# Kernel tuning notes

Hardware: AMD Instinct MI355X
Metric: run time of the kernel (lower is better)

## Reference

```python
import jax, jax.numpy as jnp
import numpy as np

# --- Mamba2Simple hyperparams (derived from init_kwargs) ---
D_MODEL = 2048
D_STATE = 128
HEADDIM = 64
EXPAND = 2
D_CONV = 4
NGROUPS = 1
CHUNK = 256
EPS = 1e-5
D_INNER = EXPAND * D_MODEL            # 4096
NHEADS = D_INNER // HEADDIM           # 64
CONV_DIM = D_INNER + 2 * NGROUPS * D_STATE          # 4352
D_IN_PROJ = 2 * D_INNER + 2 * NGROUPS * D_STATE + NHEADS  # 8512


def setup_inputs() -> dict:
    key = jax.random.key(0)
    ks = jax.random.split(key, 9)
    B, L = 2, 2048
    x = jax.random.normal(ks[0], (B, L, D_MODEL), jnp.float32)
    w_in = jax.random.normal(ks[1], (D_MODEL, D_IN_PROJ), jnp.float32) * (D_MODEL ** -0.5)
    conv_w = jax.random.normal(ks[2], (CONV_DIM, D_CONV), jnp.float32) * 0.2
    conv_b = jnp.zeros((CONV_DIM,), jnp.float32)
    dt_bias = jax.random.uniform(ks[3], (NHEADS,), jnp.float32, -4.0, -1.0)
    # A in [1, 16] per official init -> A_log = log(A)
    A_log = jnp.log(jax.random.uniform(ks[4], (NHEADS,), jnp.float32, 1.0, 16.0))
    D = jnp.ones((NHEADS,), jnp.float32)
    norm_w = jnp.ones((D_INNER,), jnp.float32)
    w_out = jax.random.normal(ks[5], (D_INNER, D_MODEL), jnp.float32) * (D_INNER ** -0.5)
    return {"x": x, "w_in": w_in, "conv_w": conv_w, "conv_b": conv_b,
            "dt_bias": dt_bias, "A_log": A_log, "D": D, "norm_w": norm_w, "w_out": w_out}


def _segsum(a):
    # a: (..., T) -> (..., T, T) with out[i, j] = sum_{k=j+1..i} a[k] for j<=i else -inf
    T = a.shape[-1]
    cs = jnp.cumsum(a, axis=-1)
    d = cs[..., :, None] - cs[..., None, :]
    mask = jnp.tril(jnp.ones((T, T), dtype=bool))
    return jnp.where(mask, d, -jnp.inf)


def _ssd(X, A, Bm, Cm):
    # X: (b, l, h, p) already multiplied by dt; A: (b, l, h) = dt*A_cont
    # Bm, Cm: (b, l, n)  (ngroups=1, broadcast over heads)
    b, l, h, p = X.shape
    n = Bm.shape[-1]
    c = l // CHUNK
    X = X.reshape(b, c, CHUNK, h, p)
    A = A.reshape(b, c, CHUNK, h).transpose(0, 3, 1, 2)      # (b, h, c, q)
    Bm = Bm.reshape(b, c, CHUNK, n)
    Cm = Cm.reshape(b, c, CHUNK, n)
    A_cs = jnp.cumsum(A, axis=-1)                             # (b, h, c, q)
    Lmat = jnp.exp(_segsum(A))                                # (b, h, c, q, q)
    # intra-chunk (diagonal block) output
    Y_diag = jnp.einsum("bcln,bcsn,bhcls,bcshp->bclhp", Cm, Bm, Lmat, X)
    # per-chunk final states
    decay_states = jnp.exp(A_cs[..., -1:] - A_cs)             # (b, h, c, q)
    states = jnp.einsum("bcln,bhcl,bclhp->bchpn", Bm, decay_states, X)
    # inter-chunk recurrence
    A_last = jnp.pad(A_cs[..., -1], ((0, 0), (0, 0), (1, 0)))  # (b, h, c+1)
    decay_chunk = jnp.exp(_segsum(A_last))                     # (b, h, c+1, c+1)
    states = jnp.concatenate([jnp.zeros_like(states[:, :1]), states], axis=1)
    states = jnp.einsum("bhzc,bchpn->bzhpn", decay_chunk, states)[:, :-1]
    # state -> output contribution
    Y_off = jnp.einsum("bchpn,bcln,bhcl->bclhp", states, Cm, jnp.exp(A_cs))
    return (Y_diag + Y_off).reshape(b, l, h, p)


def _mamba2(x, w_in, conv_w, conv_b, dt_bias, A_log, D, norm_w, w_out):
    B, L, _ = x.shape
    zxbcdt = jnp.einsum("bld,de->ble", x, w_in)               # (B, L, 8512)
    z = zxbcdt[..., :D_INNER]
    xBC = zxbcdt[..., D_INNER:D_INNER + CONV_DIM]
    dt = zxbcdt[..., D_INNER + CONV_DIM:]                      # (B, L, H)
    dt = jax.nn.softplus(dt + dt_bias)
    # causal depthwise conv1d + silu
    xp = jnp.pad(xBC, ((0, 0), (D_CONV - 1, 0), (0, 0)))
    acc = conv_b
    xBC = sum(conv_w[:, k] * xp[:, k:k + L, :] for k in range(D_CONV)) + conv_b
    xBC = jax.nn.silu(xBC)
    xh = xBC[..., :D_INNER].reshape(B, L, NHEADS, HEADDIM)
    Bm = xBC[..., D_INNER:D_INNER + NGROUPS * D_STATE]         # (B, L, N) since ngroups=1
    Cm = xBC[..., D_INNER + NGROUPS * D_STATE:]                # (B, L, N)
    A = -jnp.exp(A_log)                                        # (H,)
    y = _ssd(xh * dt[..., None], dt * A, Bm, Cm)               # (B, L, H, P)
    y = y + xh * D[None, None, :, None]                        # skip term
    y = y.reshape(B, L, D_INNER)
    # gated RMSNorm (norm_before_gate=False): normalize(y * silu(z)) * weight
    y = y * jax.nn.silu(z)
    y = y * jax.lax.rsqrt(jnp.mean(y * y, axis=-1, keepdims=True) + EPS) * norm_w
    return jnp.einsum("ble,ed->bld", y, w_out)


def reference(x, w_in, conv_w, conv_b, dt_bias, A_log, D, norm_w, w_out):
    return x + _mamba2(x, w_in, conv_w, conv_b, dt_bias, A_log, D, norm_w, w_out)
```

## Files before the change

### kernel.cpp

```cpp
#include <hip/hip_runtime.h>
#include <math.h>

#define DEV __device__ __forceinline__

typedef __attribute__((ext_vector_type(4))) float f32x4;
typedef __attribute__((ext_vector_type(4))) unsigned short u16x4;
typedef __attribute__((ext_vector_type(8))) unsigned short u16x8;
typedef __attribute__((ext_vector_type(8))) __bf16 bfv8;

DEV unsigned short f2bf(float f) {
  unsigned u = __builtin_bit_cast(unsigned, f);
  u = (u + 0x7FFFu + ((u >> 16) & 1u)) >> 16;
  return (unsigned short)u;
}
DEV float bf2f(unsigned short h) {
  unsigned u = ((unsigned)h) << 16;
  return __builtin_bit_cast(float, u);
}

DEV f32x4 mfma16(u16x8 a, u16x8 b, f32x4 c) {
  return __builtin_amdgcn_mfma_f32_16x16x32_bf16(
      __builtin_bit_cast(bfv8, a), __builtin_bit_cast(bfv8, b), c, 0, 0, 0);
}

DEV void gload_lds16(const unsigned short* g, unsigned short* s) {
  __builtin_amdgcn_global_load_lds(
      (const __attribute__((address_space(1))) void*)g,
      (__attribute__((address_space(3))) void*)s, 16, 0, 0);
}

template <int N>
DEV void vmcnt_wait() {
  if constexpr (N == 0) asm volatile("s_waitcnt vmcnt(0)" ::: "memory");
  else if constexpr (N == 2) asm volatile("s_waitcnt vmcnt(2)" ::: "memory");
  else if constexpr (N == 3) asm volatile("s_waitcnt vmcnt(3)" ::: "memory");
  else if constexpr (N == 4) asm volatile("s_waitcnt vmcnt(4)" ::: "memory");
  else if constexpr (N == 6) asm volatile("s_waitcnt vmcnt(6)" ::: "memory");
  else if constexpr (N == 8) asm volatile("s_waitcnt vmcnt(8)" ::: "memory");
}

template <int BM, int BN, int MODE>
__global__ __launch_bounds__(512, 2) void gemm_p(
    const unsigned short* __restrict__ A, const unsigned short* __restrict__ Bt,
    int K, unsigned short* __restrict__ o_z, unsigned short* __restrict__ o_xbc,
    float* __restrict__ o_dt, float* __restrict__ o_c,
    const float* __restrict__ resid) {
  constexpr int LA = BM / 128, LB = BN / 128, L = LA + LB;
  constexpr int MF = BM / 32, NF = BN / 64, MH = MF / 2;
  __shared__ __align__(16) unsigned short As[3][BM * 32];
  __shared__ __align__(16) unsigned short Bs[3][BN * 32];
  const int tid = threadIdx.x;
  const int lane = tid & 63, w = tid >> 6;
  const int l16 = lane & 15, lq = lane >> 4;
  const int wr = w >> 2, wc = w & 3;
  const int nwg = gridDim.x * gridDim.y;
  int lin = blockIdx.y * gridDim.x + blockIdx.x;
  lin = (lin & 7) * (nwg >> 3) + (lin >> 3);
  const int m0 = (lin / gridDim.x) * BM, n0 = (lin % gridDim.x) * BN;
  const int lrow = lane >> 2;
  const int gq = (lane & 3) ^ ((lrow >> 1) & 3);
  const int cq = lq ^ ((l16 >> 1) & 3);

  const unsigned short* Ag = A + (size_t)(m0 + lrow) * K + gq * 8;
  const unsigned short* Bg = Bt + (size_t)(n0 + lrow) * K + gq * 8;

  f32x4 acc[MF][NF] = {};
  u16x8 bf[NF];

  auto stageA = [&](int bi, int kt) {
#pragma unroll
    for (int i = 0; i < LA; ++i) {
      const int rb = (w + i * 8) * 16;
      gload_lds16(Ag + (size_t)rb * K + kt * 32, &As[bi][rb * 32]);
    }
  };
  auto stageB = [&](int bi, int kt) {
#pragma unroll
    for (int i = 0; i < LB; ++i) {
      const int rb = (w + i * 8) * 16;
      gload_lds16(Bg + (size_t)rb * K + kt * 32, &Bs[bi][rb * 32]);
    }
  };

  const int nt = K / 32;
  stageA(0, 0); stageB(0, 0);
  stageA(1, 1); stageB(1, 1);
  vmcnt_wait<L>();
  __builtin_amdgcn_s_barrier();

  for (int k = 0; k < nt; ++k) {
    const int cb = k % 3;
    const bool st = (k + 2) < nt;
    const int pb = st ? (k + 2) % 3 : 0;
    u16x8 af[MH];
#pragma unroll
    for (int mf = 0; mf < MH; ++mf)
      af[mf] = *(const u16x8*)(&As[cb][(wr * (BM / 2) + mf * 16 + l16) * 32 + cq * 8]);
#pragma unroll
    for (int nf = 0; nf < NF; ++nf)
      bf[nf] = *(const u16x8*)(&Bs[cb][(wc * (BN / 4) + nf * 16 + l16) * 32 + cq * 8]);
    if (st) stageA(pb, k + 2);
    asm volatile("" ::: "memory");
    __builtin_amdgcn_s_barrier();
    __builtin_amdgcn_s_setprio(1);
#pragma unroll
    for (int mf = 0; mf < MH; ++mf)
#pragma unroll
      for (int nf = 0; nf < NF; ++nf)
        acc[mf][nf] = mfma16(af[mf], bf[nf], acc[mf][nf]);
    __builtin_amdgcn_s_setprio(0);
    asm volatile("" ::: "memory");
    __builtin_amdgcn_s_barrier();
#pragma unroll
    for (int mf = 0; mf < MH; ++mf)
      af[mf] = *(const u16x8*)(&As[cb][(wr * (BM / 2) + (MH + mf) * 16 + l16) * 32 + cq * 8]);
    if (st) stageB(pb, k + 2);
    asm volatile("" ::: "memory");
    __builtin_amdgcn_s_barrier();
    __builtin_amdgcn_s_setprio(1);
#pragma unroll
    for (int mf = 0; mf < MH; ++mf)
#pragma unroll
      for (int nf = 0; nf < NF; ++nf)
        acc[MH + mf][nf] = mfma16(af[mf], bf[nf], acc[MH + mf][nf]);
    __builtin_amdgcn_s_setprio(0);
    if (k + 1 < nt) {
      if (st) vmcnt_wait<L>();
      else vmcnt_wait<0>();
    }
    asm volatile("" ::: "memory");
    __builtin_amdgcn_s_barrier();
  }

#pragma unroll
  for (int mf = 0; mf < MF; ++mf) {
#pragma unroll
    for (int nf = 0; nf < NF; ++nf) {
      const int col = n0 + wc * (BN / 4) + nf * 16 + l16;
#pragma unroll
      for (int r = 0; r < 4; ++r) {
        const int row = m0 + wr * (BM / 2) + mf * 16 + lq * 4 + r;
        float v = acc[mf][nf][r];
        if constexpr (MODE == 0) {
          if (col < 4096) o_z[(size_t)row * 4096 + col] = f2bf(v);
          else if (col < 8448) o_xbc[(size_t)row * 4352 + (col - 4096)] = f2bf(v);
          else if (col < 8512) o_dt[(size_t)row * 64 + (col - 8448)] = v;
        } else {
          size_t idx = (size_t)row * 2048 + col;
          o_c[idx] = v + resid[idx];
        }
      }
    }
  }
}

__global__ __launch_bounds__(256) void convert_bf16(
    const float* __restrict__ in, unsigned short* __restrict__ out) {
  const size_t i = ((size_t)blockIdx.x * 256 + threadIdx.x) * 8;
  f32x4 a = *(const f32x4*)(in + i);
  f32x4 b = *(const f32x4*)(in + i + 4);
  u16x8 o;
#pragma unroll
  for (int j = 0; j < 4; ++j) { o[j] = f2bf(a[j]); o[j + 4] = f2bf(b[j]); }
  *(u16x8*)(out + i) = o;
}

__global__ __launch_bounds__(256) void transpose_conv(
    const float* __restrict__ in, unsigned short* __restrict__ out, int R,
    int C) {
  __shared__ __align__(16) unsigned short T[64][72];
  const int c0 = blockIdx.x * 64, r0 = blockIdx.y * 64;
  const int tid = threadIdx.x;
#pragma unroll
  for (int it = 0; it < 4; ++it) {
    int r = it * 16 + (tid >> 4);
    int c = (tid & 15) * 4;
    f32x4 v = {0.f, 0.f, 0.f, 0.f};
    if (c0 + c < C) v = *(const f32x4*)(in + (size_t)(r0 + r) * C + c0 + c);
#pragma unroll
    for (int j = 0; j < 4; ++j) T[c + j][r] = f2bf(v[j]);
  }
  __syncthreads();
  const int nr = tid >> 2, kc = (tid & 3) * 16;
  u16x8 a = *(const u16x8*)(&T[nr][kc]);
  u16x8 b = *(const u16x8*)(&T[nr][kc + 8]);
  unsigned short* o = out + (size_t)(c0 + nr) * R + r0 + kc;
  *(u16x8*)o = a;
  *(u16x8*)(o + 8) = b;
}

__global__ __launch_bounds__(256) void conv_kernel(
    const unsigned short* __restrict__ raw, const float* __restrict__ cw,
    const float* __restrict__ cb, unsigned short* __restrict__ xbc) {
  const int ch4 = blockIdx.x * 256 + threadIdx.x;
  if (ch4 >= 1088) return;
  const int ch = ch4 * 4;
  const int row = blockIdx.y;
  const int l = row & 2047;
  f32x4 acc = *(const f32x4*)(cb + ch);
  f32x4 w0 = *(const f32x4*)(cw + ch * 4);
  f32x4 w1 = *(const f32x4*)(cw + ch * 4 + 4);
  f32x4 w2 = *(const f32x4*)(cw + ch * 4 + 8);
  f32x4 w3 = *(const f32x4*)(cw + ch * 4 + 12);
#pragma unroll
  for (int k = 0; k < 4; ++k) {
    int ls = l - 3 + k;
    if (ls >= 0) {
      u16x4 v = *(const u16x4*)(raw + (size_t)(row - 3 + k) * 4352 + ch);
      acc[0] += w0[k] * bf2f(v[0]);
      acc[1] += w1[k] * bf2f(v[1]);
      acc[2] += w2[k] * bf2f(v[2]);
      acc[3] += w3[k] * bf2f(v[3]);
    }
  }
  u16x4 o;
#pragma unroll
  for (int j = 0; j < 4; ++j) {
    float s = acc[j] / (1.0f + __expf(-acc[j]));
    o[j] = f2bf(s);
  }
  *(u16x4*)(xbc + (size_t)row * 4352 + ch) = o;
}

__global__ __launch_bounds__(256) void dt_kernel(
    float* __restrict__ dtb, const float* __restrict__ dt_bias,
    const float* __restrict__ A_log, float* __restrict__ Acs) {
  __shared__ float s[256];
  const int blk = blockIdx.x;
  const int c = blk & 7, h = (blk >> 3) & 63, b = blk >> 9;
  const int t = threadIdx.x;
  const int row = b * 2048 + c * 256 + t;
  float xv = dtb[(size_t)row * 64 + h] + dt_bias[h];
  float dt = (xv > 20.0f) ? xv : log1pf(__expf(xv));
  dtb[(size_t)row * 64 + h] = dt;
  float a = dt * (-__expf(A_log[h]));
  s[t] = a;
  __syncthreads();
  for (int off = 1; off < 256; off <<= 1) {
    float v = (t >= off) ? s[t - off] : 0.0f;
    __syncthreads();
    s[t] += v;
    __syncthreads();
  }
  Acs[((size_t)((b * 64 + h) * 8 + c)) * 256 + t] = s[t];
}

__global__ __launch_bounds__(256) void g_kernel(
    const unsigned short* __restrict__ xbc, float* __restrict__ G) {
  const int bc = blockIdx.y;
  const int i0 = (blockIdx.x >> 2) * 64, j0 = (blockIdx.x & 3) * 64;
  const int tid = threadIdx.x;
  const int lane = tid & 63, w = tid >> 6;
  const int l16 = lane & 15, lq = lane >> 4;
  const unsigned short* base = xbc + (size_t)bc * 256 * 4352;
  f32x4 acc[4] = {};
#pragma unroll
  for (int ks = 0; ks < 4; ++ks) {
    int nb = ks * 32 + lq * 8;
    u16x8 af = *(const u16x8*)(base + (size_t)(i0 + w * 16 + l16) * 4352 + 4224 + nb);
#pragma unroll
    for (int jf = 0; jf < 4; ++jf) {
      u16x8 bb = *(const u16x8*)(base + (size_t)(j0 + jf * 16 + l16) * 4352 + 4096 + nb);
      acc[jf] = mfma16(af, bb, acc[jf]);
    }
  }
  float* Gt = G + (size_t)bc * 65536;
#pragma unroll
  for (int jf = 0; jf < 4; ++jf)
#pragma unroll
    for (int r = 0; r < 4; ++r)
      Gt[(i0 + w * 16 + lq * 4 + r) * 256 + j0 + jf * 16 + l16] = acc[jf][r];
}

__global__ __launch_bounds__(512) void ssd_states(
    const unsigned short* __restrict__ xbc, const float* __restrict__ dtb,
    const float* __restrict__ Acs, unsigned short* __restrict__ statesb) {
  __shared__ __align__(16) unsigned short Xt[64 * 264];
  __shared__ __align__(16) unsigned short BmT[128 * 72];
  __shared__ float As_s[256];
  const int h = blockIdx.x, c = blockIdx.y, b = blockIdx.z;
  const int tid = threadIdx.x;
  const int lane = tid & 63, w = tid >> 6;
  const int l16 = lane & 15, lq = lane >> 4;
  const int row0 = b * 2048 + c * 256;

  if (tid < 256) As_s[tid] = Acs[((size_t)((b * 64 + h) * 8 + c)) * 256 + tid];
#pragma unroll
  for (int it = 0; it < 2; ++it) {
    int pb = tid & 15;
    int tb = it * 32 + (tid >> 4);
    float rr[4][4];
#pragma unroll
    for (int i = 0; i < 4; ++i) {
      int row = row0 + tb * 4 + i;
      u16x4 v = *(const u16x4*)(xbc + (size_t)row * 4352 + h * 64 + pb * 4);
      float dtv = dtb[(size_t)row * 64 + h];
#pragma unroll
      for (int j = 0; j < 4; ++j) rr[i][j] = bf2f(v[j]) * dtv;
    }
#pragma unroll
    for (int j = 0; j < 4; ++j) {
      u16x4 hh = {f2bf(rr[0][j]), f2bf(rr[1][j]), f2bf(rr[2][j]), f2bf(rr[3][j])};
      *(u16x4*)(&Xt[(pb * 4 + j) * 264 + tb * 4]) = hh;
    }
  }
  __syncthreads();

  f32x4 accS[4] = {};
  const float Alast = As_s[255];
  for (int part = 0; part < 4; ++part) {
    if (part) __syncthreads();
    {
      int nb = tid & 31;
      int tb = tid >> 5;
      float rr[4][4];
#pragma unroll
      for (int i = 0; i < 4; ++i) {
        int t = part * 64 + tb * 4 + i;
        int row = row0 + t;
        float dec = __expf(Alast - As_s[t]);
        u16x4 v = *(const u16x4*)(xbc + (size_t)row * 4352 + 4096 + nb * 4);
#pragma unroll
        for (int j = 0; j < 4; ++j) rr[i][j] = bf2f(v[j]) * dec;
      }
#pragma unroll
      for (int j = 0; j < 4; ++j) {
        u16x4 hh = {f2bf(rr[0][j]), f2bf(rr[1][j]), f2bf(rr[2][j]), f2bf(rr[3][j])};
        *(u16x4*)(&BmT[(nb * 4 + j) * 72 + tb * 4]) = hh;
      }
    }
    __syncthreads();
#pragma unroll
    for (int ks = 0; ks < 2; ++ks) {
      int toff = ks * 32 + lq * 8;
      u16x8 af = *(const u16x8*)(&BmT[(w * 16 + l16) * 72 + toff]);
#pragma unroll
      for (int pf = 0; pf < 4; ++pf) {
        u16x8 bfr = *(const u16x8*)(&Xt[(pf * 16 + l16) * 264 + part * 64 + toff]);
        accS[pf] = mfma16(af, bfr, accS[pf]);
      }
    }
  }
  unsigned short* Sp = statesb + (size_t)((b * 8 + c) * 64 + h) * 8192;
#pragma unroll
  for (int pf = 0; pf < 4; ++pf) {
    u16x4 hh = {f2bf(accS[pf][0]), f2bf(accS[pf][1]), f2bf(accS[pf][2]),
                f2bf(accS[pf][3])};
    *(u16x4*)(&Sp[(pf * 16 + l16) * 128 + w * 16 + lq * 4]) = hh;
  }
}

__global__ __launch_bounds__(256) void scan_states(
    const unsigned short* __restrict__ statesb, const float* __restrict__ Acs,
    unsigned short* __restrict__ prefix) {
  const int h = blockIdx.x, b = blockIdx.y;
  const int tid = threadIdx.x;
  const int p = tid >> 2, nq = (tid & 3) * 32;
  float S[32];
#pragma unroll
  for (int i = 0; i < 32; ++i) S[i] = 0.0f;
  for (int cc = 0; cc < 8; ++cc) {
    size_t base = (size_t)((b * 8 + cc) * 64 + h) * 8192 + p * 128 + nq;
#pragma unroll
    for (int j = 0; j < 4; ++j) {
      u16x8 hh;
#pragma unroll
      for (int k = 0; k < 8; ++k) hh[k] = f2bf(S[j * 8 + k]);
      *(u16x8*)(prefix + base + j * 8) = hh;
    }
    float eAl = __expf(Acs[((size_t)((b * 64 + h) * 8 + cc)) * 256 + 255]);
#pragma unroll
    for (int j = 0; j < 4; ++j) {
      u16x8 v = *(const u16x8*)(statesb + base + j * 8);
#pragma unroll
      for (int k = 0; k < 8; ++k) S[j * 8 + k] = eAl * S[j * 8 + k] + bf2f(v[k]);
    }
  }
}

__global__ __launch_bounds__(512) void ssd_main(
    const unsigned short* __restrict__ xbc, const float* __restrict__ dtb,
    const float* __restrict__ Acs, const float* __restrict__ G,
    const unsigned short* __restrict__ prefix, const float* __restrict__ Dv,
    unsigned short* __restrict__ y) {
  __shared__ __align__(16) unsigned short Xt[64 * 264];
  __shared__ float As_s[256];
  const int h = blockIdx.x, c = blockIdx.y, b = blockIdx.z;
  const int tid = threadIdx.x;
  const int lane = tid & 63, w = tid >> 6;
  const int l16 = lane & 15, lq = lane >> 4;
  const int row0 = b * 2048 + c * 256;

  if (tid < 256) As_s[tid] = Acs[((size_t)((b * 64 + h) * 8 + c)) * 256 + tid];
#pragma unroll
  for (int it = 0; it < 2; ++it) {
    int pb = tid & 15;
    int tb = it * 32 + (tid >> 4);
    float rr[4][4];
#pragma unroll
    for (int i = 0; i < 4; ++i) {
      int row = row0 + tb * 4 + i;
      u16x4 v = *(const u16x4*)(xbc + (size_t)row * 4352 + h * 64 + pb * 4);
      float dtv = dtb[(size_t)row * 64 + h];
#pragma unroll
      for (int j = 0; j < 4; ++j) rr[i][j] = bf2f(v[j]) * dtv;
    }
#pragma unroll
    for (int j = 0; j < 4; ++j) {
      u16x4 hh = {f2bf(rr[0][j]), f2bf(rr[1][j]), f2bf(rr[2][j]), f2bf(rr[3][j])};
      *(u16x4*)(&Xt[(pb * 4 + j) * 264 + tb * 4]) = hh;
    }
  }
  __syncthreads();

  f32x4 acc[2][4] = {};
  const float* Gt = G + (size_t)(b * 8 + c) * 65536;
  for (int ks = 0; ks < 8; ++ks) {
    const int tb = ks * 32 + lq * 8;
    u16x8 bfr[4];
#pragma unroll
    for (int pf = 0; pf < 4; ++pf)
      bfr[pf] = *(const u16x8*)(&Xt[(pf * 16 + l16) * 264 + tb]);
#pragma unroll
    for (int mf = 0; mf < 2; ++mf) {
      const int i = w * 32 + mf * 16 + l16;
      const float ai = As_s[i];
      const float* gp = Gt + i * 256 + tb;
      f32x4 g0 = *(const f32x4*)gp;
      f32x4 g1 = *(const f32x4*)(gp + 4);
      u16x8 af;
#pragma unroll
      for (int jj = 0; jj < 8; ++jj) {
        int j = tb + jj;
        float g = (jj < 4) ? g0[jj] : g1[jj - 4];
        float v = (i >= j) ? g * __expf(ai - As_s[j]) : 0.0f;
        af[jj] = f2bf(v);
      }
#pragma unroll
      for (int pf = 0; pf < 4; ++pf)
        acc[mf][pf] = mfma16(af, bfr[pf], acc[mf][pf]);
    }
  }
  const unsigned short* Pf = prefix + (size_t)((b * 8 + c) * 64 + h) * 8192;
  for (int ks = 0; ks < 4; ++ks) {
    const int nb = ks * 32 + lq * 8;
    u16x8 bfr[4];
#pragma unroll
    for (int pf = 0; pf < 4; ++pf)
      bfr[pf] = *(const u16x8*)(Pf + (size_t)(pf * 16 + l16) * 128 + nb);
#pragma unroll
    for (int mf = 0; mf < 2; ++mf) {
      const int i = w * 32 + mf * 16 + l16;
      const float eAi = __expf(As_s[i]);
      u16x8 cv = *(const u16x8*)(xbc + (size_t)(row0 + i) * 4352 + 4224 + nb);
      u16x8 af;
#pragma unroll
      for (int jj = 0; jj < 8; ++jj) af[jj] = f2bf(bf2f(cv[jj]) * eAi);
#pragma unroll
      for (int pf = 0; pf < 4; ++pf)
        acc[mf][pf] = mfma16(af, bfr[pf], acc[mf][pf]);
    }
  }
  const float Dh = Dv[h];
#pragma unroll
  for (int mf = 0; mf < 2; ++mf) {
#pragma unroll
    for (int r = 0; r < 4; ++r) {
      int t = w * 32 + mf * 16 + lq * 4 + r;
      size_t row = (size_t)(row0 + t);
#pragma unroll
      for (int pf = 0; pf < 4; ++pf) {
        int p = pf * 16 + l16;
        float xh = bf2f(xbc[row * 4352 + h * 64 + p]);
        y[row * 4096 + h * 64 + p] = f2bf(acc[mf][pf][r] + Dh * xh);
      }
    }
  }
}

__global__ __launch_bounds__(256) void norm_kernel(
    unsigned short* __restrict__ y, const unsigned short* __restrict__ zbf,
    const float* __restrict__ nw) {
  const int row = blockIdx.x, tid = threadIdx.x;
  unsigned short* yr = y + (size_t)row * 4096;
  const unsigned short* zr = zbf + (size_t)row * 4096;
  float vals[16];
  float ss = 0.0f;
#pragma unroll
  for (int i = 0; i < 2; ++i) {
    int cb = i * 2048 + tid * 8;
    u16x8 yv = *(const u16x8*)(yr + cb);
    u16x8 zv = *(const u16x8*)(zr + cb);
#pragma unroll
    for (int j = 0; j < 8; ++j) {
      float z = bf2f(zv[j]);
      float g = bf2f(yv[j]) * (z / (1.0f + __expf(-z)));
      vals[i * 8 + j] = g;
      ss += g * g;
    }
  }
#pragma unroll
  for (int off = 32; off > 0; off >>= 1) ss += __shfl_xor(ss, off, 64);
  __shared__ float red[4];
  if ((tid & 63) == 0) red[tid >> 6] = ss;
  __syncthreads();
  float tot = red[0] + red[1] + red[2] + red[3];
  float rr = rsqrtf(tot * (1.0f / 4096.0f) + 1e-5f);
#pragma unroll
  for (int i = 0; i < 2; ++i) {
    int cb = i * 2048 + tid * 8;
    f32x4 w0 = *(const f32x4*)(nw + cb);
    f32x4 w1 = *(const f32x4*)(nw + cb + 4);
    u16x8 o;
#pragma unroll
    for (int j = 0; j < 8; ++j) {
      float wv = (j < 4) ? w0[j] : w1[j - 4];
      o[j] = f2bf(vals[i * 8 + j] * rr * wv);
    }
    *(u16x8*)(yr + cb) = o;
  }
}

extern "C" void kernel_launch(void* const* d_in, const int* in_sizes, int n_in,
                              void* d_out, int out_size, void* d_ws,
                              size_t ws_size, hipStream_t stream) {
  const float* x = (const float*)d_in[0];
  const float* w_in = (const float*)d_in[1];
  const float* conv_w = (const float*)d_in[2];
  const float* conv_b = (const float*)d_in[3];
  const float* dt_bias = (const float*)d_in[4];
  const float* A_log = (const float*)d_in[5];
  const float* Dvec = (const float*)d_in[6];
  const float* norm_w = (const float*)d_in[7];
  const float* w_out = (const float*)d_in[8];
  float* out = (float*)d_out;

  char* w = (char*)d_ws;
  unsigned short* zbf = (unsigned short*)(w + 0);
  unsigned short* xbc = (unsigned short*)(w + 33554432);
  unsigned short* xbcraw = (unsigned short*)(w + 69206016);
  float* dtb = (float*)(w + 104857600);
  float* Acs = (float*)(w + 105906176);
  float* G = (float*)(w + 106954752);
  unsigned short* statesb = (unsigned short*)(w + 111149056);
  unsigned short* y = (unsigned short*)(w + 127926272);
  unsigned short* xbf = (unsigned short*)(w + 111149056);
  unsigned short* w_inT = (unsigned short*)(w + 33554432);
  unsigned short* w_outT = (unsigned short*)(w + 33554432);
  unsigned short* prefix = xbcraw;

  convert_bf16<<<dim3(4096), 256, 0, stream>>>(x, xbf);
  transpose_conv<<<dim3(136, 32), 256, 0, stream>>>(w_in, w_inT, 2048, 8512);
  gemm_p<256, 256, 0><<<dim3(34, 16), 512, 0, stream>>>(
      xbf, w_inT, 2048, zbf, xbcraw, dtb, nullptr, nullptr);
  conv_kernel<<<dim3(5, 4096), 256, 0, stream>>>(xbcraw, conv_w, conv_b, xbc);
  dt_kernel<<<dim3(1024), 256, 0, stream>>>(dtb, dt_bias, A_log, Acs);
  g_kernel<<<dim3(16, 16), 256, 0, stream>>>(xbc, G);
  ssd_states<<<dim3(64, 8, 2), 512, 0, stream>>>(xbc, dtb, Acs, statesb);
  scan_states<<<dim3(64, 2), 256, 0, stream>>>(statesb, Acs, prefix);
  ssd_main<<<dim3(64, 8, 2), 512, 0, stream>>>(xbc, dtb, Acs, G, prefix, Dvec, y);
  transpose_conv<<<dim3(32, 64), 256, 0, stream>>>(w_out, w_outT, 4096, 2048);
  norm_kernel<<<dim3(4096), 256, 0, stream>>>(y, zbf, norm_w);
  gemm_p<128, 128, 1><<<dim3(16, 32), 512, 0, stream>>>(
      y, w_outT, 4096, nullptr, nullptr, nullptr, out, x);
}
```

Measured before the change: 503.4 us.

## Simplify GEMM pipeline to one barrier per k-step and widen out-proj tile

Reworks the GEMM main loop so each k-iteration uses a single vmcnt wait and barrier, issues the prefetch of both A and B tiles for k+2 at once, and loads all A fragments before the MFMA bursts, replacing the four-barrier split schedule. It also changes the output projection GEMM tile from 128x128 to 128x256, halving its grid. The goal is less synchronisation overhead and better B reuse per workgroup. The trade-offs are more registers for the full A fragment set, less interleaving of loads with MFMAs, and fewer workgroups (256) for the out-proj on a many-CU device.

```diff
diff --git a/kernel.cpp b/kernel.cpp
--- a/kernel.cpp
+++ b/kernel.cpp
@@ -65,16 +65,13 @@
   const unsigned short* Bg = Bt + (size_t)(n0 + lrow) * K + gq * 8;
 
   f32x4 acc[MF][NF] = {};
-  u16x8 bf[NF];
-
-  auto stageA = [&](int bi, int kt) {
+
+  auto stage = [&](int bi, int kt) {
 #pragma unroll
     for (int i = 0; i < LA; ++i) {
       const int rb = (w + i * 8) * 16;
       gload_lds16(Ag + (size_t)rb * K + kt * 32, &As[bi][rb * 32]);
     }
-  };
-  auto stageB = [&](int bi, int kt) {
 #pragma unroll
     for (int i = 0; i < LB; ++i) {
       const int rb = (w + i * 8) * 16;
@@ -83,25 +80,27 @@
   };
 
   const int nt = K / 32;
-  stageA(0, 0); stageB(0, 0);
-  stageA(1, 1); stageB(1, 1);
-  vmcnt_wait<L>();
-  __builtin_amdgcn_s_barrier();
+  stage(0, 0);
+  stage(1, 1);
 
   for (int k = 0; k < nt; ++k) {
     const int cb = k % 3;
-    const bool st = (k + 2) < nt;
-    const int pb = st ? (k + 2) % 3 : 0;
-    u16x8 af[MH];
+    if (k < nt - 1) vmcnt_wait<L>();
+    else vmcnt_wait<0>();
+    __builtin_amdgcn_s_barrier();
+    if (k + 2 < nt) stage((k + 2) % 3, k + 2);
+
+    u16x8 af[MF], bf[NF];
 #pragma unroll
     for (int mf = 0; mf < MH; ++mf)
       af[mf] = *(const u16x8*)(&As[cb][(wr * (BM / 2) + mf * 16 + l16) * 32 + cq * 8]);
 #pragma unroll
     for (int nf = 0; nf < NF; ++nf)
       bf[nf] = *(const u16x8*)(&Bs[cb][(wc * (BN / 4) + nf * 16 + l16) * 32 + cq * 8]);
-    if (st) stageA(pb, k + 2);
-    asm volatile("" ::: "memory");
-    __builtin_amdgcn_s_barrier();
+#pragma unroll
+    for (int mf = MH; mf < MF; ++mf)
+      af[mf] = *(const u16x8*)(&As[cb][(wr * (BM / 2) + mf * 16 + l16) * 32 + cq * 8]);
+
     __builtin_amdgcn_s_setprio(1);
 #pragma unroll
     for (int mf = 0; mf < MH; ++mf)
@@ -109,27 +108,13 @@
       for (int nf = 0; nf < NF; ++nf)
         acc[mf][nf] = mfma16(af[mf], bf[nf], acc[mf][nf]);
     __builtin_amdgcn_s_setprio(0);
-    asm volatile("" ::: "memory");
-    __builtin_amdgcn_s_barrier();
-#pragma unroll
-    for (int mf = 0; mf < MH; ++mf)
-      af[mf] = *(const u16x8*)(&As[cb][(wr * (BM / 2) + (MH + mf) * 16 + l16) * 32 + cq * 8]);
-    if (st) stageB(pb, k + 2);
-    asm volatile("" ::: "memory");
-    __builtin_amdgcn_s_barrier();
     __builtin_amdgcn_s_setprio(1);
 #pragma unroll
-    for (int mf = 0; mf < MH; ++mf)
+    for (int mf = MH; mf < MF; ++mf)
 #pragma unroll
       for (int nf = 0; nf < NF; ++nf)
-        acc[MH + mf][nf] = mfma16(af[mf], bf[nf], acc[MH + mf][nf]);
+        acc[mf][nf] = mfma16(af[mf], bf[nf], acc[mf][nf]);
     __builtin_amdgcn_s_setprio(0);
-    if (k + 1 < nt) {
-      if (st) vmcnt_wait<L>();
-      else vmcnt_wait<0>();
-    }
-    asm volatile("" ::: "memory");
-    __builtin_amdgcn_s_barrier();
   }
 
 #pragma unroll
@@ -561,6 +546,6 @@
   ssd_main<<<dim3(64, 8, 2), 512, 0, stream>>>(xbc, dtb, Acs, G, prefix, Dvec, y);
   transpose_conv<<<dim3(32, 64), 256, 0, stream>>>(w_out, w_outT, 4096, 2048);
   norm_kernel<<<dim3(4096), 256, 0, stream>>>(y, zbf, norm_w);
-  gemm_p<128, 128, 1><<<dim3(16, 32), 512, 0, stream>>>(
+  gemm_p<128, 256, 1><<<dim3(8, 32), 512, 0, stream>>>(
       y, w_outT, 4096, nullptr, nullptr, nullptr, out, x);
 }
```

Result: slower. 574.0 us (+14.0%).
